# Kernel tuning notes

Hardware: AMD Instinct MI355X
Metric: run time of the kernel (lower is better)

The kernel has to match this reference:

```python
import jax, jax.numpy as jnp
import numpy as np

ALPHA = 1.0
MIN_FEATURE_SIZE = 1.0
SC = 1e-12
EPS_V_FLOOR = 1e-32 ** (1.0 / 6.0)  # ~4.64e-6, floor on gradient magnitude


def setup_inputs() -> dict:
    key = jax.random.key(0)
    eps = jax.random.normal(key, (8192, 8192), dtype=jnp.float32)
    grid_size = jnp.asarray(0.05, dtype=jnp.float32)
    return {"eps": eps, "grid_size": grid_size}


def _ls_derivatives(phi, d):
    # torch.gradient == numpy.gradient with edge_order=1 (central interior, one-sided edges)
    phi_x, phi_y = jnp.gradient(phi, d, d)
    phi_x = phi_x + SC
    phi_y = phi_y + SC
    phi_xx, phi_xy = jnp.gradient(phi_x, d, d)        # second derivs of phi_x
    phi_yy = jnp.gradient(phi_y, d, axis=1)           # only d/dy of phi_y is used
    return phi_x, phi_y, phi_xx, phi_xy, phi_yy


def reference(eps, grid_size):
    ex, ey, exx, exy, eyy = _ls_derivatives(eps, grid_size)
    pi_d = jnp.pi / (1.1 * MIN_FEATURE_SIZE)
    eps_v = jnp.maximum(jnp.sqrt(ex * ex + ey * ey), jnp.float32(EPS_V_FLOOR))
    k = (ex * ex * eyy - 2.0 * ex * ey * exy + ey * ey * exx) / (eps_v ** 3)
    curve_const = jnp.abs(k * jnp.arctan(eps_v / (eps + 1e-6))) - pi_d
    return jnp.nansum(ALPHA * jnp.maximum(curve_const, 0.0) * grid_size ** 2)
```

## Files before the change

kernel.cpp:

```cpp
#include <hip/hip_runtime.h>
#include <math.h>


typedef float f2 __attribute__((ext_vector_type(2)));
typedef float f4 __attribute__((ext_vector_type(4)));

constexpr float SCF = 1e-12f;
constexpr float EVF = 4.6415888336e-6f;
constexpr float PID = 2.8559933214452666f;
constexpr float PIH = 1.5707963268f;
constexpr int   RS  = 64;

struct Row { f4 lo, hi; };

__device__ __forceinline__ float C(const Row& r, int k) {
    return k < 4 ? r.lo[k] : r.hi[k - 4];
}
__device__ __forceinline__ void load_row(Row& r, const float* p) {
    r.lo = *(const f4*)p;
    r.hi = *(const f4*)(p + 4);
}
__device__ __forceinline__ f2 mk(float a, float b) { f2 v; v.x = a; v.y = b; return v; }
__device__ __forceinline__ f2 fma2(f2 a, f2 b, f2 c) { return __builtin_elementwise_fma(a, b, c); }
__device__ __forceinline__ f2 max2(f2 a, f2 b) { return __builtin_elementwise_max(a, b); }
__device__ __forceinline__ f2 min2(f2 a, f2 b) { return __builtin_elementwise_min(a, b); }
__device__ __forceinline__ f2 abs2(f2 a) { return __builtin_elementwise_abs(a); }
__device__ __forceinline__ f2 rcp2(f2 a) {
    return mk(__builtin_amdgcn_rcpf(a.x), __builtin_amdgcn_rcpf(a.y));
}
__device__ __forceinline__ f2 rsq2(f2 a) {
    return mk(__builtin_amdgcn_rsqf(a.x), __builtin_amdgcn_rsqf(a.y));
}

__device__ __forceinline__ f2 compute_pair(const Row& R0, const Row& R1,
                                           const Row& R2, const Row& R3,
                                           const Row& R4, const Row& R5,
                                           f2 inv2d, f2 inv4dd) {
    f2 dif[6];
    #pragma unroll
    for (int k = 0; k < 6; ++k)
        dif[k] = mk(C(R3, k + 1) - C(R1, k + 1),
                    C(R4, k + 1) - C(R2, k + 1));
    f2 Pz[8];
    #pragma unroll
    for (int k = 0; k < 8; ++k)
        Pz[k] = mk(C(R2, k), C(R3, k));

    const f2 sc2 = mk(SCF, SCF);
    f2 part = mk(0.0f, 0.0f);
    #pragma unroll
    for (int q = 0; q < 4; ++q) {
        const f2 c00 = Pz[q + 2];
        const f2 ex  = fma2(dif[q + 1], inv2d, sc2);
        const f2 ey  = fma2(Pz[q + 3] - Pz[q + 1], inv2d, sc2);
        const f2 sxx = mk(C(R4, q + 2) + C(R0, q + 2),
                          C(R5, q + 2) + C(R1, q + 2));
        const f2 exx = (sxx - 2.0f * c00) * inv4dd;
        const f2 eyy = (Pz[q + 4] + Pz[q] - 2.0f * c00) * inv4dd;
        const f2 exy = (dif[q + 2] - dif[q]) * inv4dd;

        const f2 s2  = fma2(ex, ex, ey * ey);
        const f2 rsq = rsq2(s2);
        const f2 ev  = max2(s2 * rsq, mk(EVF, EVF));
        const f2 iv3 = min2(rsq * rsq * rsq, mk(1e16f, 1e16f));
        const f2 num = fma2(ex * ex, eyy,
                       fma2(-2.0f * (ex * ey), exy, (ey * ey) * exx));
        const f2 kabs = abs2(num) * iv3;

        const f2 aw = abs2(c00 + 1e-6f);
        const f2 mx = max2(ev, aw);
        const f2 mn = min2(ev, aw);
        const f2 t  = mn * rcp2(mx);
        const f2 t2 = t * t;
        f2 pl = fma2(t2, mk(-0.01172120f, -0.01172120f), mk(0.05265332f, 0.05265332f));
        pl = fma2(t2, pl, mk(-0.11643287f, -0.11643287f));
        pl = fma2(t2, pl, mk(0.19354346f, 0.19354346f));
        pl = fma2(t2, pl, mk(-0.33262347f, -0.33262347f));
        pl = fma2(t2, pl, mk(0.99997726f, 0.99997726f));
        pl = pl * t;
        f2 at;
        at.x = (ev.x > aw.x) ? PIH - pl.x : pl.x;
        at.y = (ev.y > aw.y) ? PIH - pl.y : pl.y;

        part = part + max2(fma2(kabs, at, mk(-PID, -PID)), mk(0.0f, 0.0f));
    }
    return part;
}

__device__ __forceinline__ float eg(const float* __restrict__ e, int n, int i, int j) {
    return e[(size_t)i * (size_t)n + j];
}
__device__ __forceinline__ float gex(const float* __restrict__ e, int n, int i, int j,
                                     float inv_d, float inv_2d) {
    float v;
    if (i == 0)          v = (eg(e, n, 1, j) - eg(e, n, 0, j)) * inv_d;
    else if (i == n - 1) v = (eg(e, n, n - 1, j) - eg(e, n, n - 2, j)) * inv_d;
    else                 v = (eg(e, n, i + 1, j) - eg(e, n, i - 1, j)) * inv_2d;
    return v + SCF;
}
__device__ __forceinline__ float gey(const float* __restrict__ e, int n, int i, int j,
                                     float inv_d, float inv_2d) {
    float v;
    if (j == 0)          v = (eg(e, n, i, 1) - eg(e, n, i, 0)) * inv_d;
    else if (j == n - 1) v = (eg(e, n, i, n - 1) - eg(e, n, i, n - 2)) * inv_d;
    else                 v = (eg(e, n, i, j + 1) - eg(e, n, i, j - 1)) * inv_2d;
    return v + SCF;
}

__global__ __launch_bounds__(256, 4)
void fab_fused(const float* __restrict__ eps, const float* __restrict__ gs,
               float* __restrict__ ws, int n, int G2, int nfr) {
    const float d       = *gs;
    const float inv_2d  = 0.5f / d;
    const float inv_4dd = inv_2d * inv_2d;

    float acc = 0.0f;

    if (threadIdx.x < 96) {
        const int bflat = blockIdx.y * gridDim.x + blockIdx.x;
        const int idx = bflat * 96 + (int)threadIdx.x;
        if (idx < nfr) {
            const float inv_d = inv_2d + inv_2d;
            int i, j;
            if (idx < 4 * n) {
                const int rr = (idx >= n) + (idx >= 2 * n) + (idx >= 3 * n);
                j = idx - rr * n;
                i = (rr < 2) ? rr : (n - 4) + rr;
            } else {
                const int t = idx - 4 * n;
                i = 2 + (t >> 3);
                const int cc = t & 7;
                j = (cc < 2) ? cc : (n - 8) + cc;
            }

            const float ex0 = gex(eps, n, i, j, inv_d, inv_2d);
            const float ey0 = gey(eps, n, i, j, inv_d, inv_2d);

            float exx, exy, eyy;
            if (i == 0)
                exx = (gex(eps, n, 1, j, inv_d, inv_2d) - ex0) * inv_d;
            else if (i == n - 1)
                exx = (ex0 - gex(eps, n, n - 2, j, inv_d, inv_2d)) * inv_d;
            else
                exx = (gex(eps, n, i + 1, j, inv_d, inv_2d)
                     - gex(eps, n, i - 1, j, inv_d, inv_2d)) * inv_2d;

            if (j == 0)
                exy = (gex(eps, n, i, 1, inv_d, inv_2d) - ex0) * inv_d;
            else if (j == n - 1)
                exy = (ex0 - gex(eps, n, i, n - 2, inv_d, inv_2d)) * inv_d;
            else
                exy = (gex(eps, n, i, j + 1, inv_d, inv_2d)
                     - gex(eps, n, i, j - 1, inv_d, inv_2d)) * inv_2d;

            if (j == 0)
                eyy = (gey(eps, n, i, 1, inv_d, inv_2d) - ey0) * inv_d;
            else if (j == n - 1)
                eyy = (ey0 - gey(eps, n, i, n - 2, inv_d, inv_2d)) * inv_d;
            else
                eyy = (gey(eps, n, i, j + 1, inv_d, inv_2d)
                     - gey(eps, n, i, j - 1, inv_d, inv_2d)) * inv_2d;

            const float ev = fmaxf(__builtin_amdgcn_sqrtf(fmaf(ex0, ex0, ey0 * ey0)), EVF);
            const float num = fmaf(ex0 * ex0, eyy,
                              fmaf(-2.0f * ex0 * ey0, exy, ey0 * ey0 * exx));
            const float kabs = fabsf(num) * __builtin_amdgcn_rcpf(ev * ev * ev);

            const float aw = fabsf(eg(eps, n, i, j) + 1e-6f);
            const float mx = fmaxf(ev, aw);
            const float mn = fminf(ev, aw);
            const float t  = mn * __builtin_amdgcn_rcpf(mx);
            const float t2 = t * t;
            float pl = fmaf(t2, -0.01172120f, 0.05265332f);
            pl = fmaf(t2, pl, -0.11643287f);
            pl = fmaf(t2, pl, 0.19354346f);
            pl = fmaf(t2, pl, -0.33262347f);
            pl = fmaf(t2, pl, 0.99997726f);
            pl *= t;
            const float at = (ev > aw) ? (PIH - pl) : pl;

            acc += fmaxf(fmaf(kabs, at, -PID), 0.0f);
        }
    }

    {
        const int gg = blockIdx.x * 256 + threadIdx.x;
        const bool valid = gg < G2;
        const int gc = min(gg, G2 - 1);
        const int i0 = 2 + RS * blockIdx.y;
        const int count = min(RS, (n - 2) - i0);
        const float*  pj = eps + 4 * (size_t)gc;
        const size_t  sn = (size_t)n;
        const f2 inv2d2  = mk(inv_2d, inv_2d);
        const f2 inv4dd2 = mk(inv_4dd, inv_4dd);

        Row s0, s1, s2, s3, s4, s5, s6, s7;
        load_row(s0, pj + (size_t)(i0 - 2) * sn);
        load_row(s1, pj + (size_t)(i0 - 1) * sn);
        load_row(s2, pj + (size_t)(i0    ) * sn);
        load_row(s3, pj + (size_t)(i0 + 1) * sn);
        load_row(s4, pj + (size_t)(i0 + 2) * sn);
        load_row(s5, pj + (size_t)(i0 + 3) * sn);
        const float* pnext = pj + (size_t)(i0 + 4) * sn;

        f2 acc2 = mk(0.0f, 0.0f);
        #define PHASEP(ph, A0, A1, A2, A3, A4, A5, L0, L1)                    \
        {                                                                     \
            const int k = kbase + 2 * (ph);                                   \
            if (k < count) {                                                  \
                if (k + 2 < count) {                                          \
                    load_row(L0, pnext);                                      \
                    load_row(L1, pnext + sn);                                 \
                }                                                             \
                pnext += 2 * sn;                                              \
                acc2 = acc2 + compute_pair(A0, A1, A2, A3, A4, A5,            \
                                           inv2d2, inv4dd2);                  \
            }                                                                 \
        }

        #pragma unroll 1
        for (int kbase = 0; kbase < RS; kbase += 8) {
            PHASEP(0, s0, s1, s2, s3, s4, s5, s6, s7)
            PHASEP(1, s2, s3, s4, s5, s6, s7, s0, s1)
            PHASEP(2, s4, s5, s6, s7, s0, s1, s2, s3)
            PHASEP(3, s6, s7, s0, s1, s2, s3, s4, s5)
        }
        #undef PHASEP

        if (valid) acc += acc2.x + acc2.y;
    }

    __shared__ float wsum[4];
    #pragma unroll
    for (int off = 32; off; off >>= 1)
        acc += __shfl_down(acc, off, 64);
    if ((threadIdx.x & 63) == 0) wsum[threadIdx.x >> 6] = acc;
    __syncthreads();
    if (threadIdx.x == 0) {
        const int slot = (blockIdx.y * gridDim.x + blockIdx.x) & 63;
        atomicAdd(&ws[slot], wsum[0] + wsum[1] + wsum[2] + wsum[3]);
    }
}

__global__ __launch_bounds__(64)
void fab_finish(const float* __restrict__ ws, const float* __restrict__ gs,
                float* __restrict__ out) {
    const float d = *gs;
    float v = ws[threadIdx.x];
    #pragma unroll
    for (int off = 32; off; off >>= 1)
        v += __shfl_down(v, off, 64);
    if (threadIdx.x == 0) out[0] = v * d * d;
}

extern "C" void kernel_launch(void* const* d_in, const int* in_sizes, int n_in,
                              void* d_out, int out_size, void* d_ws, size_t ws_size,
                              hipStream_t stream) {
    const float* eps = (const float*)d_in[0];
    const float* gs  = (const float*)d_in[1];
    float* out = (float*)d_out;
    float* ws  = (float*)d_ws;

    const long long tot = (long long)in_sizes[0];
    const int n = (int)(sqrt((double)tot) + 0.5);

    hipMemsetAsync(ws, 0, 64 * sizeof(float), stream);

    const int G2  = (n - 8) / 4;
    const int nstrip = (n - 4 + RS - 1) / RS;
    const int nfr = 4 * n + 8 * (n - 4);

    dim3 block(256, 1);
    dim3 grid(n / 1024, nstrip);
    fab_fused<<<grid, block, 0, stream>>>(eps, gs, ws, n, G2, nfr);
    fab_finish<<<1, 64, 0, stream>>>(ws, gs, out);
}
```

Before: 94.46 us.

## Fold derivative scale factors into curvature, hoist row loads, drop memset and atomics

The curvature is rewritten in terms of raw finite differences, with the 1/(2d) scale factors folded into two constants applied at the end. This removes per-element multiplies, and the SC offset is dropped as negligible. The initial strip row loads are moved ahead of the frame-edge work so their latency overlaps it. The per-block atomic slot accumulation and the memset launch are replaced by plain per-block writes, and a 256-thread finish kernel sums all block partials. Dropping SC and reordering the scaling could change results slightly near degenerate gradients.

```diff
diff --git a/kernel.cpp b/kernel.cpp
--- a/kernel.cpp
+++ b/kernel.cpp
@@ -35,7 +35,7 @@
 __device__ __forceinline__ f2 compute_pair(const Row& R0, const Row& R1,
                                            const Row& R2, const Row& R3,
                                            const Row& R4, const Row& R5,
-                                           f2 inv2d, f2 inv4dd) {
+                                           f2 c1, f2 c2) {
     f2 dif[6];
     #pragma unroll
     for (int k = 0; k < 6; ++k)
@@ -46,26 +46,26 @@
     for (int k = 0; k < 8; ++k)
         Pz[k] = mk(C(R2, k), C(R3, k));
 
-    const f2 sc2 = mk(SCF, SCF);
     f2 part = mk(0.0f, 0.0f);
     #pragma unroll
     for (int q = 0; q < 4; ++q) {
-        const f2 c00 = Pz[q + 2];
-        const f2 ex  = fma2(dif[q + 1], inv2d, sc2);
-        const f2 ey  = fma2(Pz[q + 3] - Pz[q + 1], inv2d, sc2);
-        const f2 sxx = mk(C(R4, q + 2) + C(R0, q + 2),
-                          C(R5, q + 2) + C(R1, q + 2));
-        const f2 exx = (sxx - 2.0f * c00) * inv4dd;
-        const f2 eyy = (Pz[q + 4] + Pz[q] - 2.0f * c00) * inv4dd;
-        const f2 exy = (dif[q + 2] - dif[q]) * inv4dd;
-
-        const f2 s2  = fma2(ex, ex, ey * ey);
-        const f2 rsq = rsq2(s2);
-        const f2 ev  = max2(s2 * rsq, mk(EVF, EVF));
-        const f2 iv3 = min2(rsq * rsq * rsq, mk(1e16f, 1e16f));
-        const f2 num = fma2(ex * ex, eyy,
-                       fma2(-2.0f * (ex * ey), exy, (ey * ey) * exx));
-        const f2 kabs = abs2(num) * iv3;
+        const f2 c00  = Pz[q + 2];
+        const f2 u    = dif[q + 1];
+        const f2 v    = Pz[q + 3] - Pz[q + 1];
+        const f2 exxr = fma2(mk(-2.0f, -2.0f), c00,
+                             mk(C(R4, q + 2) + C(R0, q + 2),
+                                C(R5, q + 2) + C(R1, q + 2)));
+        const f2 eyyr = fma2(mk(-2.0f, -2.0f), c00, Pz[q + 4] + Pz[q]);
+        const f2 exyr = dif[q + 2] - dif[q];
+
+        const f2 uu  = u * u;
+        const f2 vv  = v * v;
+        const f2 r2  = uu + vv;
+        const f2 rsq = rsq2(r2);
+        const f2 N   = fma2(uu, eyyr, fma2(-2.0f * (u * v), exyr, vv * exxr));
+        const f2 r3  = rsq * rsq * rsq;
+        const f2 kabs = abs2(N) * min2(c1 * r3, c2);
+        const f2 ev   = max2(c1 * (r2 * rsq), mk(EVF, EVF));
 
         const f2 aw = abs2(c00 + 1e-6f);
         const f2 mx = max2(ev, aw);
@@ -110,11 +110,29 @@
 __global__ __launch_bounds__(256, 4)
 void fab_fused(const float* __restrict__ eps, const float* __restrict__ gs,
                float* __restrict__ ws, int n, int G2, int nfr) {
-    const float d       = *gs;
-    const float inv_2d  = 0.5f / d;
-    const float inv_4dd = inv_2d * inv_2d;
+    const float d      = *gs;
+    const float inv_2d = 0.5f / d;
+    const float c1s    = inv_2d;
+    const float c2s    = 1e16f * (inv_2d * inv_2d) * (inv_2d * inv_2d);
 
     float acc = 0.0f;
+
+    const int gg = blockIdx.x * 256 + threadIdx.x;
+    const bool valid = gg < G2;
+    const int gc = min(gg, G2 - 1);
+    const int i0 = 2 + RS * blockIdx.y;
+    const int count = min(RS, (n - 2) - i0);
+    const float*  pj = eps + 4 * (size_t)gc;
+    const size_t  sn = (size_t)n;
+
+    Row s0, s1, s2, s3, s4, s5, s6, s7;
+    load_row(s0, pj + (size_t)(i0 - 2) * sn);
+    load_row(s1, pj + (size_t)(i0 - 1) * sn);
+    load_row(s2, pj + (size_t)(i0    ) * sn);
+    load_row(s3, pj + (size_t)(i0 + 1) * sn);
+    load_row(s4, pj + (size_t)(i0 + 2) * sn);
+    load_row(s5, pj + (size_t)(i0 + 3) * sn);
+    const float* pnext = pj + (size_t)(i0 + 4) * sn;
 
     if (threadIdx.x < 96) {
         const int bflat = blockIdx.y * gridDim.x + blockIdx.x;
@@ -184,24 +202,8 @@
     }
 
     {
-        const int gg = blockIdx.x * 256 + threadIdx.x;
-        const bool valid = gg < G2;
-        const int gc = min(gg, G2 - 1);
-        const int i0 = 2 + RS * blockIdx.y;
-        const int count = min(RS, (n - 2) - i0);
-        const float*  pj = eps + 4 * (size_t)gc;
-        const size_t  sn = (size_t)n;
-        const f2 inv2d2  = mk(inv_2d, inv_2d);
-        const f2 inv4dd2 = mk(inv_4dd, inv_4dd);
-
-        Row s0, s1, s2, s3, s4, s5, s6, s7;
-        load_row(s0, pj + (size_t)(i0 - 2) * sn);
-        load_row(s1, pj + (size_t)(i0 - 1) * sn);
-        load_row(s2, pj + (size_t)(i0    ) * sn);
-        load_row(s3, pj + (size_t)(i0 + 1) * sn);
-        load_row(s4, pj + (size_t)(i0 + 2) * sn);
-        load_row(s5, pj + (size_t)(i0 + 3) * sn);
-        const float* pnext = pj + (size_t)(i0 + 4) * sn;
+        const f2 c1 = mk(c1s, c1s);
+        const f2 c2 = mk(c2s, c2s);
 
         f2 acc2 = mk(0.0f, 0.0f);
         #define PHASEP(ph, A0, A1, A2, A3, A4, A5, L0, L1)                    \
@@ -213,8 +215,7 @@
                     load_row(L1, pnext + sn);                                 \
                 }                                                             \
                 pnext += 2 * sn;                                              \
-                acc2 = acc2 + compute_pair(A0, A1, A2, A3, A4, A5,            \
-                                           inv2d2, inv4dd2);                  \
+                acc2 = acc2 + compute_pair(A0, A1, A2, A3, A4, A5, c1, c2);   \
             }                                                                 \
         }
 
@@ -236,21 +237,26 @@
         acc += __shfl_down(acc, off, 64);
     if ((threadIdx.x & 63) == 0) wsum[threadIdx.x >> 6] = acc;
     __syncthreads();
-    if (threadIdx.x == 0) {
-        const int slot = (blockIdx.y * gridDim.x + blockIdx.x) & 63;
-        atomicAdd(&ws[slot], wsum[0] + wsum[1] + wsum[2] + wsum[3]);
-    }
-}
-
-__global__ __launch_bounds__(64)
+    if (threadIdx.x == 0)
+        ws[blockIdx.y * gridDim.x + blockIdx.x] =
+            wsum[0] + wsum[1] + wsum[2] + wsum[3];
+}
+
+__global__ __launch_bounds__(256)
 void fab_finish(const float* __restrict__ ws, const float* __restrict__ gs,
-                float* __restrict__ out) {
-    const float d = *gs;
-    float v = ws[threadIdx.x];
+                float* __restrict__ out, int nb) {
+    __shared__ float wsum[4];
+    float v = 0.0f;
+    for (int i = threadIdx.x; i < nb; i += 256) v += ws[i];
     #pragma unroll
     for (int off = 32; off; off >>= 1)
         v += __shfl_down(v, off, 64);
-    if (threadIdx.x == 0) out[0] = v * d * d;
+    if ((threadIdx.x & 63) == 0) wsum[threadIdx.x >> 6] = v;
+    __syncthreads();
+    if (threadIdx.x == 0) {
+        const float d = *gs;
+        out[0] = (wsum[0] + wsum[1] + wsum[2] + wsum[3]) * d * d;
+    }
 }
 
 extern "C" void kernel_launch(void* const* d_in, const int* in_sizes, int n_in,
@@ -264,8 +270,6 @@
     const long long tot = (long long)in_sizes[0];
     const int n = (int)(sqrt((double)tot) + 0.5);
 
-    hipMemsetAsync(ws, 0, 64 * sizeof(float), stream);
-
     const int G2  = (n - 8) / 4;
     const int nstrip = (n - 4 + RS - 1) / RS;
     const int nfr = 4 * n + 8 * (n - 4);
@@ -273,5 +277,5 @@
     dim3 block(256, 1);
     dim3 grid(n / 1024, nstrip);
     fab_fused<<<grid, block, 0, stream>>>(eps, gs, ws, n, G2, nfr);
-    fab_finish<<<1, 64, 0, stream>>>(ws, gs, out);
-}
+    fab_finish<<<1, 256, 0, stream>>>(ws, gs, out, grid.x * grid.y);
+}
```

New measurement: 90.47 us. 4.2% less time.
